# Kernel tuning notes

Measured on AMD Instinct MI355X. Metric: run time of the kernel, lower is better.

Reference implementation:

```python
import jax, jax.numpy as jnp
import numpy as np

B, T, I, H, L, C = 256, 128, 256, 1024, 2, 1000


def setup_inputs() -> dict:
    key = jax.random.key(0)
    ks = jax.random.split(key, 11)
    s_ih = 1.0 / np.sqrt(H)
    inp = {
        "x": jax.random.normal(ks[0], (B, T, I), dtype=jnp.float32),
        # layer 0: input_size -> hidden
        "Wih0": jax.random.uniform(ks[1], (H, I), jnp.float32, -s_ih, s_ih),
        "Whh0": jax.random.uniform(ks[2], (H, H), jnp.float32, -s_ih, s_ih),
        "bih0": jax.random.uniform(ks[3], (H,), jnp.float32, -s_ih, s_ih),
        "bhh0": jax.random.uniform(ks[4], (H,), jnp.float32, -s_ih, s_ih),
        # layer 1: hidden -> hidden
        "Wih1": jax.random.uniform(ks[5], (H, H), jnp.float32, -s_ih, s_ih),
        "Whh1": jax.random.uniform(ks[6], (H, H), jnp.float32, -s_ih, s_ih),
        "bih1": jax.random.uniform(ks[7], (H,), jnp.float32, -s_ih, s_ih),
        "bhh1": jax.random.uniform(ks[8], (H,), jnp.float32, -s_ih, s_ih),
        # fc head
        "fcW": jax.random.uniform(ks[9], (C, H), jnp.float32, -s_ih, s_ih),
        "fcb": jax.random.uniform(ks[10], (C,), jnp.float32, -s_ih, s_ih),
    }
    return inp


def _rnn_layer(x, Wih, Whh, bih, bhh):
    # x: [B, T, in]; h_t = tanh(x_t Wih^T + bih + h_{t-1} Whh^T + bhh)
    b, t, _ = x.shape
    h0 = jnp.zeros((b, Whh.shape[0]), dtype=x.dtype)
    # precompute input projection for all timesteps in one big GEMM
    xp = jnp.einsum('bti,hi->tbh', x, Wih) + (bih + bhh)  # [T, B, H]

    def step(h, xp_t):
        h_new = jnp.tanh(xp_t + h @ Whh.T)
        return h_new, h_new

    _, hs = jax.lax.scan(step, h0, xp)  # hs: [T, B, H]
    return jnp.transpose(hs, (1, 0, 2))  # [B, T, H]


def reference(x, Wih0, Whh0, bih0, bhh0, Wih1, Whh1, bih1, bhh1, fcW, fcb):
    x = jnp.reshape(x, (-1, T, I))
    h1 = _rnn_layer(x, Wih0, Whh0, bih0, bhh0)
    h2 = _rnn_layer(h1, Wih1, Whh1, bih1, bhh1)
    last = h2[:, -1, :]  # [B, H]
    return last @ fcW.T + fcb  # [B, C]
```

## Files before the change

kernel.cpp:

```cpp
#include <hip/hip_runtime.h>
#include <hip/hip_bf16.h>
#include <cstdint>
#include <cstddef>

typedef short v8s __attribute__((ext_vector_type(8)));
typedef float v4f __attribute__((ext_vector_type(4)));
typedef float v16f __attribute__((ext_vector_type(16)));

#define TT 128
#define BB 256
#define HH 1024
#define II 256
#define CC 1000

#define OFF_WHH0 0u
#define OFF_WHH1 1048576u
#define OFF_WIH1 2097152u
#define OFF_WIH0 3145728u
#define WSW_SHORTS 3407872u

#define NJ 32
#define CSTR 64
#define CNT_UINTS (12 * CSTR)
#define CNT_BYTES (CNT_UINTS * 4)

#define NCHUNK_LDS 50

__device__ __forceinline__ unsigned short f2bf(float f) {
  unsigned int u = __float_as_uint(f);
  u += 0x7fffu + ((u >> 16) & 1u);
  return (unsigned short)(u >> 16);
}
__device__ __forceinline__ float bf2f(unsigned short s) {
  return __uint_as_float((unsigned int)s << 16);
}
__device__ __forceinline__ float fast_tanh(float x) {
  float ax = fabsf(x);
  float e = __expf(-2.0f * ax);
  float r = 1.0f - 2.0f * e / (1.0f + e);
  return x < 0.0f ? -r : r;
}
__device__ __forceinline__ v16f mfma32(v8s a, v8s b, v16f c) {
  return __builtin_amdgcn_mfma_f32_32x32x16_bf16(a, b, c, 0, 0, 0);
}

__device__ __forceinline__ void poll_cnt(const unsigned int* p, unsigned int need) {
  while (__hip_atomic_load(p, __ATOMIC_RELAXED, __HIP_MEMORY_SCOPE_AGENT) < need)
    __builtin_amdgcn_s_sleep(1);
}
__device__ __forceinline__ void spin_tok(int* tok, int need) {
  while (__hip_atomic_load(tok, __ATOMIC_ACQUIRE, __HIP_MEMORY_SCOPE_WORKGROUP) < need) {}
  asm volatile("" ::: "memory");
}
__device__ __forceinline__ void set_tok(int* tok, int v) {
  __hip_atomic_store(tok, v, __ATOMIC_RELEASE, __HIP_MEMORY_SCOPE_WORKGROUP);
}
__device__ __forceinline__ void store16_llc(unsigned short* addr, v8s val) {
  asm volatile("global_store_dwordx4 %0, %1, off sc0 sc1"
               :: "v"(addr), "v"(val) : "memory");
}
__device__ __forceinline__ void waitcnt_vm0() {
  asm volatile("s_waitcnt vmcnt(0)" ::: "memory");
}

__global__ void swizzle_w(const float* __restrict__ W, unsigned short* __restrict__ out,
                          int K, int total) {
  int idx = blockIdx.x * 256 + threadIdx.x;
  if (idx >= total) return;
  int lane = idx & 63;
  int rest = idx >> 6;
  int KC = K >> 4;
  int kk = rest & (KC - 1);
  int jt = rest / KC;
  int row = jt * 32 + (lane & 31);
  int k0 = kk * 16 + (lane >> 5) * 8;
  const float* src = W + (size_t)row * K + k0;
  float4 f0 = *(const float4*)src;
  float4 f1 = *(const float4*)(src + 4);
  unsigned short o[8] = {f2bf(f0.x), f2bf(f0.y), f2bf(f0.z), f2bf(f0.w),
                         f2bf(f1.x), f2bf(f1.y), f2bf(f1.z), f2bf(f1.w)};
  *(v8s*)(out + (size_t)idx * 8) = *(const v8s*)o;
}

__global__ __launch_bounds__(256, 1) void xp_kernel(
    const float* __restrict__ x, const unsigned short* __restrict__ wih_sw,
    const float* __restrict__ bih0, const float* __restrict__ bhh0,
    unsigned short* __restrict__ xp) {
  __shared__ unsigned short lA[16 * 64 * 8];
  const int tid = threadIdx.x;
  const int lane = tid & 63, wave = tid >> 6;
  const int bi = blockIdx.x;
  const int t = bi >> 3, g = (bi >> 1) & 3, tile = bi & 1;
  const int b0 = g * 64 + tile * 32;
  #pragma unroll
  for (int s = 0; s < 4; ++s) {
    int idx = s * 256 + tid;
    int row = idx >> 5, kg = idx & 31;
    const float* src = x + ((size_t)(b0 + row) * TT + t) * II + kg * 8;
    float4 f0 = *(const float4*)src;
    float4 f1 = *(const float4*)(src + 4);
    unsigned short o[8] = {f2bf(f0.x), f2bf(f0.y), f2bf(f0.z), f2bf(f0.w),
                           f2bf(f1.x), f2bf(f1.y), f2bf(f1.z), f2bf(f1.w)};
    int kk = kg >> 1, hf = kg & 1;
    *(v8s*)(lA + ((size_t)kk * 64 + hf * 32 + row) * 8) = *(const v8s*)o;
  }
  __syncthreads();
  const int col = lane & 31;
  for (int jj = 0; jj < 8; ++jj) {
    int jt = wave * 8 + jj;
    float bias = bih0[jt * 32 + col] + bhh0[jt * 32 + col];
    v16f acc;
    #pragma unroll
    for (int r = 0; r < 16; ++r) acc[r] = bias;
    const unsigned short* bw = wih_sw + (size_t)jt * 8192;
    #pragma unroll 4
    for (int kk = 0; kk < 16; ++kk) {
      v8s a = *(const v8s*)(lA + ((size_t)kk * 64 + lane) * 8);
      v8s b = *(const v8s*)(bw + ((size_t)kk * 64 + lane) * 8);
      acc = mfma32(a, b, acc);
    }
    unsigned short o[16];
    #pragma unroll
    for (int r = 0; r < 16; ++r) o[r] = f2bf(acc[r]);
    unsigned short* dst = xp + ((size_t)((t * 4 + g) * 32 + jt) * 2 + tile) * 1024 + lane * 16;
    *(v8s*)dst = *(const v8s*)o;
    *(v8s*)(dst + 8) = *(const v8s*)(o + 8);
  }
}

template <int XPON, int BIGH2>
__global__ __launch_bounds__(256, 1) void rnn_fused(
    const float* __restrict__ x, const unsigned short* __restrict__ wsw,
    const unsigned short* __restrict__ xp,
    const float* __restrict__ bih0, const float* __restrict__ bhh0,
    const float* __restrict__ bih1, const float* __restrict__ bhh1,
    unsigned short* __restrict__ hbuf, unsigned short* __restrict__ h2buf,
    unsigned int* cnt) {
  __shared__ unsigned short lds_whh[NCHUNK_LDS * 512];
  __shared__ float lds_acc[2 * 1024];
  __shared__ unsigned short lds_pack[64 * 40];
  __shared__ int tok[4];

  const int tid = threadIdx.x;
  const int xsel = blockIdx.x & 7;
  const int layer = xsel >> 2;
  const int g = xsel & 3;
  const int jt = blockIdx.x >> 3;
  const int lane = tid & 63;
  const int wave = tid >> 6;
  const int tile = wave & 1;
  const int kh = wave >> 1;
  const int col = lane & 31;
  const int half = lane >> 5;
  const int j0 = jt * 32;

  const unsigned short* whh_tile =
      wsw + (layer ? OFF_WHH1 : OFF_WHH0) + (size_t)jt * 32768;
  const unsigned short* wih_tile =
      layer ? (wsw + OFF_WIH1 + (size_t)jt * 32768)
            : (wsw + OFF_WIH0 + (size_t)jt * 8192);

  for (int i = tid * 8; i < NCHUNK_LDS * 512; i += 2048)
    *(v8s*)(lds_whh + i) = *(const v8s*)(whh_tile + i);

  float bias = 0.0f;
  if (layer == 1) bias = bih1[j0 + col] + bhh1[j0 + col];
  else if (!XPON) bias = bih0[j0 + col] + bhh0[j0 + col];
  if (tid < 4) tok[tid] = 0;
  __syncthreads();

  const int arow = g * 64 + tile * 32 + col;
  unsigned int* cntA_g = cnt + (size_t)(0 * 4 + g) * CSTR;
  unsigned int* cntX_g = cnt + (size_t)(1 * 4 + g) * CSTR;
  unsigned int* cntB_g = cnt + (size_t)(2 * 4 + g) * CSTR;

  v8s xc0 = {}, xc1 = {};
  const unsigned short* xpb =
      xp + (((size_t)g * 32 + jt) * 2 + tile) * 1024 + lane * 16;
  if (XPON && layer == 0 && kh == 0) {
    xc0 = *(const v8s*)xpb;
    xc1 = *(const v8s*)(xpb + 8);
  }

  auto bL = [&](int kk) -> v8s {
    return *(const v8s*)(lds_whh + ((size_t)kk * 64 + lane) * 8);
  };
  auto bG = [&](int kk) -> v8s {
    return *(const v8s*)(whh_tile + ((size_t)kk * 64 + lane) * 8);
  };
  auto bI = [&](int kk) -> v8s {
    return *(const v8s*)(wih_tile + ((size_t)kk * 64 + lane) * 8);
  };

  for (int t = 0; t < TT; ++t) {
    v16f acc = {};

    if (layer == 0) {
      if (kh == 0) {
        if (XPON) {
          union { v8s v[2]; unsigned short u[16]; } xu;
          xu.v[0] = xc0; xu.v[1] = xc1;
          #pragma unroll
          for (int r = 0; r < 16; ++r) acc[r] = bf2f(xu.u[r]);
        } else {
          #pragma unroll
          for (int r = 0; r < 16; ++r) acc[r] = bias;
          const float* xr = x + ((size_t)arow * TT + t) * II + half * 8;
          #pragma unroll 4
          for (int kk = 0; kk < 16; ++kk) {
            float4 f0 = *(const float4*)(xr + kk * 16);
            float4 f1 = *(const float4*)(xr + kk * 16 + 4);
            unsigned short o[8] = {f2bf(f0.x), f2bf(f0.y), f2bf(f0.z), f2bf(f0.w),
                                   f2bf(f1.x), f2bf(f1.y), f2bf(f1.z), f2bf(f1.w)};
            acc = mfma32(*(const v8s*)o, bI(kk), acc);
          }
        }
        if (t > 0) {
          if (wave == 0) { poll_cnt(cntA_g, 32u * (unsigned)t); set_tok(&tok[0], t); }
          else           { spin_tok(&tok[0], t); }
          const unsigned short* hr = hbuf + ((size_t)t * BB + arow) * HH + half * 8;
          v8s aA[16], aB[16];
          #pragma unroll
          for (int kk = 0; kk < 16; ++kk) aA[kk] = *(const v8s*)(hr + kk * 16);
          #pragma unroll
          for (int kk = 0; kk < 16; ++kk) aB[kk] = *(const v8s*)(hr + (16 + kk) * 16);
          #pragma unroll
          for (int kk = 0; kk < 16; ++kk) acc = mfma32(aA[kk], bL(kk), acc);
          #pragma unroll
          for (int kk = 0; kk < 16; ++kk) acc = mfma32(aB[kk], bL(16 + kk), acc);
        }
        if (XPON) {
          int tn = (t + 1 < TT) ? (t + 1) : (TT - 1);
          const unsigned short* nx = xpb + (size_t)tn * 262144;
          xc0 = *(const v8s*)nx;
          xc1 = *(const v8s*)(nx + 8);
        }
      } else {
        if (t > 0) {
          spin_tok(&tok[0], t);
          const unsigned short* hr = hbuf + ((size_t)t * BB + arow) * HH + half * 8;
          v8s aA[16], aB[16];
          #pragma unroll
          for (int kk = 0; kk < 16; ++kk) aA[kk] = *(const v8s*)(hr + (32 + kk) * 16);
          #pragma unroll
          for (int kk = 0; kk < 16; ++kk) aB[kk] = *(const v8s*)(hr + (48 + kk) * 16);
          #pragma unroll
          for (int kk = 0; kk < 16; ++kk) {
            v8s b = (32 + kk < NCHUNK_LDS) ? bL(32 + kk) : bG(32 + kk);
            acc = mfma32(aA[kk], b, acc);
          }
          #pragma unroll
          for (int kk = 0; kk < 16; ++kk) {
            v8s b = (48 + kk < NCHUNK_LDS) ? bL(48 + kk) : bG(48 + kk);
            acc = mfma32(aB[kk], b, acc);
          }
        }
      }
    } else {
      if (kh == 0) {
        #pragma unroll
        for (int r = 0; r < 16; ++r) acc[r] = bias;
        if (wave == 0) { poll_cnt(cntX_g, 32u * (unsigned)(t + 1)); set_tok(&tok[1], t + 1); }
        else           { spin_tok(&tok[1], t + 1); }
        const unsigned short* hr = hbuf + ((size_t)(t + 1) * BB + arow) * HH + half * 8;
        v8s aA[16], aB[16];
        #pragma unroll
        for (int kk = 0; kk < 16; ++kk) aA[kk] = *(const v8s*)(hr + kk * 16);
        #pragma unroll
        for (int kk = 0; kk < 16; ++kk) aB[kk] = *(const v8s*)(hr + (16 + kk) * 16);
        #pragma unroll
        for (int kk = 0; kk < 16; ++kk) acc = mfma32(aA[kk], bI(kk), acc);
        #pragma unroll
        for (int kk = 0; kk < 16; ++kk) aA[kk] = *(const v8s*)(hr + (32 + kk) * 16);
        #pragma unroll
        for (int kk = 0; kk < 16; ++kk) acc = mfma32(aB[kk], bI(16 + kk), acc);
        #pragma unroll
        for (int kk = 0; kk < 16; ++kk) aB[kk] = *(const v8s*)(hr + (48 + kk) * 16);
        #pragma unroll
        for (int kk = 0; kk < 16; ++kk) acc = mfma32(aA[kk], bI(32 + kk), acc);
        #pragma unroll
        for (int kk = 0; kk < 16; ++kk) acc = mfma32(aB[kk], bI(48 + kk), acc);
      } else {
        if (t > 0) {
          if (wave == 2) { poll_cnt(cntB_g, 32u * (unsigned)t); set_tok(&tok[2], t); }
          else           { spin_tok(&tok[2], t); }
          const int slot_r = BIGH2 ? (t - 1) : ((t - 1) & 1);
          const unsigned short* hr =
              h2buf + ((size_t)slot_r * BB + arow) * HH + half * 8;
          if (BIGH2) {
            v8s aA[16], aB[16];
            #pragma unroll
            for (int kk = 0; kk < 16; ++kk) aA[kk] = *(const v8s*)(hr + kk * 16);
            #pragma unroll
            for (int kk = 0; kk < 16; ++kk) aB[kk] = *(const v8s*)(hr + (16 + kk) * 16);
            #pragma unroll
            for (int kk = 0; kk < 16; ++kk) acc = mfma32(aA[kk], bL(kk), acc);
            #pragma unroll
            for (int kk = 0; kk < 16; ++kk) aA[kk] = *(const v8s*)(hr + (32 + kk) * 16);
            #pragma unroll
            for (int kk = 0; kk < 16; ++kk) acc = mfma32(aB[kk], bL(16 + kk), acc);
            #pragma unroll
            for (int kk = 0; kk < 16; ++kk) aB[kk] = *(const v8s*)(hr + (48 + kk) * 16);
            #pragma unroll
            for (int kk = 0; kk < 16; ++kk) {
              v8s b = (32 + kk < NCHUNK_LDS) ? bL(32 + kk) : bG(32 + kk);
              acc = mfma32(aA[kk], b, acc);
            }
            #pragma unroll
            for (int kk = 0; kk < 16; ++kk) {
              v8s b = (48 + kk < NCHUNK_LDS) ? bL(48 + kk) : bG(48 + kk);
              acc = mfma32(aB[kk], b, acc);
            }
          } else {
            #pragma unroll 8
            for (int kk = 0; kk < 64; ++kk) {
              const unsigned long long* p = (const unsigned long long*)(hr + kk * 16);
              unsigned long long lo = __hip_atomic_load(p, __ATOMIC_RELAXED, __HIP_MEMORY_SCOPE_AGENT);
              unsigned long long hi = __hip_atomic_load(p + 1, __ATOMIC_RELAXED, __HIP_MEMORY_SCOPE_AGENT);
              union { unsigned long long q[2]; v8s v; } u;
              u.q[0] = lo; u.q[1] = hi;
              v8s b = (kk < NCHUNK_LDS) ? bL(kk) : bG(kk);
              acc = mfma32(u.v, b, acc);
            }
          }
        }
      }
    }

    if (kh == 1) {
      float* dst = lds_acc + tile * 1024;
      #pragma unroll
      for (int r4 = 0; r4 < 4; ++r4)
        *(float4*)(dst + r4 * 256 + lane * 4) =
            make_float4(acc[r4 * 4], acc[r4 * 4 + 1], acc[r4 * 4 + 2], acc[r4 * 4 + 3]);
    }
    __syncthreads();

    if (kh == 0) {
      const float* srcp = lds_acc + tile * 1024;
      #pragma unroll
      for (int r4 = 0; r4 < 4; ++r4) {
        float4 part = *(const float4*)(srcp + r4 * 256 + lane * 4);
        float pv[4] = {part.x, part.y, part.z, part.w};
        #pragma unroll
        for (int q = 0; q < 4; ++q) {
          int r = r4 * 4 + q;
          int row_l = tile * 32 + q + 8 * r4 + 4 * half;
          lds_pack[row_l * 40 + col] = f2bf(fast_tanh(acc[r] + pv[q]));
        }
      }
    }
    __syncthreads();

    {
      int row_l = tid >> 2, cg = tid & 3;
      v8s hv = *(const v8s*)(lds_pack + row_l * 40 + cg * 8);
      int slot_w = layer ? (BIGH2 ? t : (t & 1)) : (t + 1);
      unsigned short* hout = (layer ? h2buf : hbuf) +
          ((size_t)slot_w * BB + g * 64 + row_l) * HH + j0 + cg * 8;
      store16_llc(hout, hv);
    }
    waitcnt_vm0();
    __syncthreads();
    if (tid == 0) {
      if (layer == 0) {
        __hip_atomic_fetch_add(cntA_g, 1u, __ATOMIC_RELAXED, __HIP_MEMORY_SCOPE_AGENT);
        __hip_atomic_fetch_add(cntX_g, 1u, __ATOMIC_RELAXED, __HIP_MEMORY_SCOPE_AGENT);
      } else {
        __hip_atomic_fetch_add(cntB_g, 1u, __ATOMIC_RELAXED, __HIP_MEMORY_SCOPE_AGENT);
      }
    }
  }
}

__global__ __launch_bounds__(256, 1) void fc_kernel(
    const unsigned short* __restrict__ h2, const float* __restrict__ fcW,
    const float* __restrict__ fcb, float* __restrict__ out) {
  const int tid = threadIdx.x;
  const int ct = blockIdx.x % 63;
  const int g = blockIdx.x / 63;
  const int lane = tid & 63;
  const int wave = tid >> 6;
  const int n = lane & 15;
  const int quad = lane >> 4;
  const int c = ct * 16 + n;
  const int cs = c < CC ? c : CC - 1;
  const float bias = fcb[cs];
  v4f acc = {bias, bias, bias, bias};
  const unsigned short* hr = h2 + (size_t)(g * 64 + wave * 16 + n) * HH + quad * 8;
  const float* wr = fcW + (size_t)cs * HH + quad * 8;
  #pragma unroll 8
  for (int kk = 0; kk < HH / 32; ++kk) {
    v8s a = *(const v8s*)(hr + kk * 32);
    float4 f0 = *(const float4*)(wr + kk * 32);
    float4 f1 = *(const float4*)(wr + kk * 32 + 4);
    v8s b;
    b[0] = (short)f2bf(f0.x); b[1] = (short)f2bf(f0.y);
    b[2] = (short)f2bf(f0.z); b[3] = (short)f2bf(f0.w);
    b[4] = (short)f2bf(f1.x); b[5] = (short)f2bf(f1.y);
    b[6] = (short)f2bf(f1.z); b[7] = (short)f2bf(f1.w);
    acc = __builtin_amdgcn_mfma_f32_16x16x32_bf16(a, b, acc, 0, 0, 0);
  }
  if (c < CC) {
    const int b0 = g * 64 + wave * 16 + quad * 4;
    #pragma unroll
    for (int i = 0; i < 4; ++i) out[(size_t)(b0 + i) * CC + c] = acc[i];
  }
}

extern "C" void kernel_launch(void* const* d_in, const int* in_sizes, int n_in,
                              void* d_out, int out_size, void* d_ws, size_t ws_size,
                              hipStream_t stream) {
  (void)in_sizes; (void)n_in; (void)out_size;
  const float* x    = (const float*)d_in[0];
  const float* Wih0 = (const float*)d_in[1];
  const float* Whh0 = (const float*)d_in[2];
  const float* bih0 = (const float*)d_in[3];
  const float* bhh0 = (const float*)d_in[4];
  const float* Wih1 = (const float*)d_in[5];
  const float* Whh1 = (const float*)d_in[6];
  const float* bih1 = (const float*)d_in[7];
  const float* bhh1 = (const float*)d_in[8];
  const float* fcW  = (const float*)d_in[9];
  const float* fcb  = (const float*)d_in[10];

  const size_t hbuf_elems = (size_t)(TT + 1) * BB * HH;
  const size_t h2_full = (size_t)TT * BB * HH;
  const size_t h2_par  = (size_t)2 * BB * HH;
  const size_t xp_elems = (size_t)TT * BB * HH;

  const size_t needA = (WSW_SHORTS + hbuf_elems + h2_full + xp_elems) * 2 + CNT_BYTES;
  const size_t needB = (WSW_SHORTS + hbuf_elems + h2_par + xp_elems) * 2 + CNT_BYTES;
  const bool tierA = ws_size >= needA;
  const bool tierB = !tierA && ws_size >= needB;

  unsigned short* wsw = (unsigned short*)d_ws;
  unsigned short* hbuf = wsw + WSW_SHORTS;
  unsigned short* h2buf = hbuf + hbuf_elems;
  unsigned short* xpbuf = h2buf + (tierA ? h2_full : h2_par);
  unsigned int* cnt = (unsigned int*)(xpbuf + ((tierA || tierB) ? xp_elems : 0));

  hipMemsetAsync(cnt, 0, CNT_BYTES, stream);
  swizzle_w<<<512, 256, 0, stream>>>(Whh0, wsw + OFF_WHH0, HH, 32 * 64 * 64);
  swizzle_w<<<512, 256, 0, stream>>>(Whh1, wsw + OFF_WHH1, HH, 32 * 64 * 64);
  swizzle_w<<<512, 256, 0, stream>>>(Wih1, wsw + OFF_WIH1, HH, 32 * 64 * 64);
  swizzle_w<<<128, 256, 0, stream>>>(Wih0, wsw + OFF_WIH0, II, 32 * 16 * 64);

  if (tierA || tierB)
    xp_kernel<<<1024, 256, 0, stream>>>(x, wsw + OFF_WIH0, bih0, bhh0, xpbuf);

  if (tierA) {
    rnn_fused<1, 1><<<256, 256, 0, stream>>>(
        x, wsw, xpbuf, bih0, bhh0, bih1, bhh1, hbuf, h2buf, cnt);
  } else if (tierB) {
    rnn_fused<1, 0><<<256, 256, 0, stream>>>(
        x, wsw, xpbuf, bih0, bhh0, bih1, bhh1, hbuf, h2buf, cnt);
  } else {
    rnn_fused<0, 0><<<256, 256, 0, stream>>>(
        x, wsw, xpbuf, bih0, bhh0, bih1, bhh1, hbuf, h2buf, cnt);
  }

  const unsigned short* h2last = h2buf + (size_t)(tierA ? (TT - 1) : 1) * BB * HH;
  fc_kernel<<<63 * 4, 256, 0, stream>>>(h2last, fcW, fcb, (float*)d_out);
}
```

Measured before the change: 1.665 ms.

## Per-wave counter signaling, batched hidden-state loads, and sched_group_barrier MFMA interleave

```diff
diff --git a/kernel.cpp b/kernel.cpp
--- a/kernel.cpp
+++ b/kernel.cpp
@@ -25,6 +25,15 @@
 #define CNT_BYTES (CNT_UINTS * 4)
 
 #define NCHUNK_LDS 50
+
+#if defined(__has_builtin)
+#if __has_builtin(__builtin_amdgcn_sched_group_barrier)
+#define SGB(m, n) __builtin_amdgcn_sched_group_barrier((m), (n), 0)
+#endif
+#endif
+#ifndef SGB
+#define SGB(m, n)
+#endif
 
 __device__ __forceinline__ unsigned short f2bf(float f) {
   unsigned int u = __float_as_uint(f);
@@ -202,6 +211,10 @@
           xu.v[0] = xc0; xu.v[1] = xc1;
           #pragma unroll
           for (int r = 0; r < 16; ++r) acc[r] = bf2f(xu.u[r]);
+          int tn = (t + 1 < TT) ? (t + 1) : (TT - 1);
+          const unsigned short* nx = xpb + (size_t)tn * 262144;
+          xc0 = *(const v8s*)nx;
+          xc1 = *(const v8s*)(nx + 8);
         } else {
           #pragma unroll
           for (int r = 0; r < 16; ++r) acc[r] = bias;
@@ -216,101 +229,77 @@
           }
         }
         if (t > 0) {
-          if (wave == 0) { poll_cnt(cntA_g, 32u * (unsigned)t); set_tok(&tok[0], t); }
+          if (wave == 0) { poll_cnt(cntA_g, 128u * (unsigned)t); set_tok(&tok[0], t); }
           else           { spin_tok(&tok[0], t); }
           const unsigned short* hr = hbuf + ((size_t)t * BB + arow) * HH + half * 8;
-          v8s aA[16], aB[16];
-          #pragma unroll
-          for (int kk = 0; kk < 16; ++kk) aA[kk] = *(const v8s*)(hr + kk * 16);
-          #pragma unroll
-          for (int kk = 0; kk < 16; ++kk) aB[kk] = *(const v8s*)(hr + (16 + kk) * 16);
-          #pragma unroll
-          for (int kk = 0; kk < 16; ++kk) acc = mfma32(aA[kk], bL(kk), acc);
-          #pragma unroll
-          for (int kk = 0; kk < 16; ++kk) acc = mfma32(aB[kk], bL(16 + kk), acc);
-        }
-        if (XPON) {
-          int tn = (t + 1 < TT) ? (t + 1) : (TT - 1);
-          const unsigned short* nx = xpb + (size_t)tn * 262144;
-          xc0 = *(const v8s*)nx;
-          xc1 = *(const v8s*)(nx + 8);
+          v8s ar[32];
+          #pragma unroll
+          for (int kk = 0; kk < 32; ++kk) ar[kk] = *(const v8s*)(hr + kk * 16);
+          #pragma unroll
+          for (int kk = 0; kk < 32; ++kk) acc = mfma32(ar[kk], bL(kk), acc);
+          SGB(0x20, 32);
+          SGB(0x108, 64);
         }
       } else {
         if (t > 0) {
           spin_tok(&tok[0], t);
           const unsigned short* hr = hbuf + ((size_t)t * BB + arow) * HH + half * 8;
-          v8s aA[16], aB[16];
-          #pragma unroll
-          for (int kk = 0; kk < 16; ++kk) aA[kk] = *(const v8s*)(hr + (32 + kk) * 16);
-          #pragma unroll
-          for (int kk = 0; kk < 16; ++kk) aB[kk] = *(const v8s*)(hr + (48 + kk) * 16);
-          #pragma unroll
-          for (int kk = 0; kk < 16; ++kk) {
+          v8s ar[32];
+          #pragma unroll
+          for (int kk = 0; kk < 32; ++kk) ar[kk] = *(const v8s*)(hr + (32 + kk) * 16);
+          #pragma unroll
+          for (int kk = 0; kk < 32; ++kk) {
             v8s b = (32 + kk < NCHUNK_LDS) ? bL(32 + kk) : bG(32 + kk);
-            acc = mfma32(aA[kk], b, acc);
+            acc = mfma32(ar[kk], b, acc);
           }
-          #pragma unroll
-          for (int kk = 0; kk < 16; ++kk) {
-            v8s b = (48 + kk < NCHUNK_LDS) ? bL(48 + kk) : bG(48 + kk);
-            acc = mfma32(aB[kk], b, acc);
-          }
+          SGB(0x20, 46);
+          SGB(0x108, 50);
         }
       }
     } else {
       if (kh == 0) {
         #pragma unroll
         for (int r = 0; r < 16; ++r) acc[r] = bias;
-        if (wave == 0) { poll_cnt(cntX_g, 32u * (unsigned)(t + 1)); set_tok(&tok[1], t + 1); }
+        if (wave == 0) { poll_cnt(cntX_g, 128u * (unsigned)(t + 1)); set_tok(&tok[1], t + 1); }
         else           { spin_tok(&tok[1], t + 1); }
         const unsigned short* hr = hbuf + ((size_t)(t + 1) * BB + arow) * HH + half * 8;
-        v8s aA[16], aB[16];
-        #pragma unroll
-        for (int kk = 0; kk < 16; ++kk) aA[kk] = *(const v8s*)(hr + kk * 16);
-        #pragma unroll
-        for (int kk = 0; kk < 16; ++kk) aB[kk] = *(const v8s*)(hr + (16 + kk) * 16);
-        #pragma unroll
-        for (int kk = 0; kk < 16; ++kk) acc = mfma32(aA[kk], bI(kk), acc);
-        #pragma unroll
-        for (int kk = 0; kk < 16; ++kk) aA[kk] = *(const v8s*)(hr + (32 + kk) * 16);
-        #pragma unroll
-        for (int kk = 0; kk < 16; ++kk) acc = mfma32(aB[kk], bI(16 + kk), acc);
-        #pragma unroll
-        for (int kk = 0; kk < 16; ++kk) aB[kk] = *(const v8s*)(hr + (48 + kk) * 16);
-        #pragma unroll
-        for (int kk = 0; kk < 16; ++kk) acc = mfma32(aA[kk], bI(32 + kk), acc);
-        #pragma unroll
-        for (int kk = 0; kk < 16; ++kk) acc = mfma32(aB[kk], bI(48 + kk), acc);
+        v8s ar[32];
+        #pragma unroll
+        for (int kk = 0; kk < 32; ++kk) ar[kk] = *(const v8s*)(hr + kk * 16);
+        #pragma unroll
+        for (int kk = 0; kk < 32; ++kk) acc = mfma32(ar[kk], bI(kk), acc);
+        SGB(0x20, 64);
+        SGB(0x8, 32);
+        #pragma unroll
+        for (int kk = 0; kk < 32; ++kk) ar[kk] = *(const v8s*)(hr + (32 + kk) * 16);
+        #pragma unroll
+        for (int kk = 0; kk < 32; ++kk) acc = mfma32(ar[kk], bI(32 + kk), acc);
+        SGB(0x20, 64);
+        SGB(0x8, 32);
       } else {
         if (t > 0) {
-          if (wave == 2) { poll_cnt(cntB_g, 32u * (unsigned)t); set_tok(&tok[2], t); }
+          if (wave == 2) { poll_cnt(cntB_g, 128u * (unsigned)t); set_tok(&tok[2], t); }
           else           { spin_tok(&tok[2], t); }
           const int slot_r = BIGH2 ? (t - 1) : ((t - 1) & 1);
           const unsigned short* hr =
               h2buf + ((size_t)slot_r * BB + arow) * HH + half * 8;
           if (BIGH2) {
-            v8s aA[16], aB[16];
+            v8s ar[32];
             #pragma unroll
-            for (int kk = 0; kk < 16; ++kk) aA[kk] = *(const v8s*)(hr + kk * 16);
+            for (int kk = 0; kk < 32; ++kk) ar[kk] = *(const v8s*)(hr + kk * 16);
             #pragma unroll
-            for (int kk = 0; kk < 16; ++kk) aB[kk] = *(const v8s*)(hr + (16 + kk) * 16);
+            for (int kk = 0; kk < 32; ++kk) acc = mfma32(ar[kk], bL(kk), acc);
+            SGB(0x20, 32);
+            SGB(0x108, 64);
             #pragma unroll
-            for (int kk = 0; kk < 16; ++kk) acc = mfma32(aA[kk], bL(kk), acc);
+            for (int kk = 0; kk < 32; ++kk) ar[kk] = *(const v8s*)(hr + (32 + kk) * 16);
             #pragma unroll
-            for (int kk = 0; kk < 16; ++kk) aA[kk] = *(const v8s*)(hr + (32 + kk) * 16);
-            #pragma unroll
-            for (int kk = 0; kk < 16; ++kk) acc = mfma32(aB[kk], bL(16 + kk), acc);
-            #pragma unroll
-            for (int kk = 0; kk < 16; ++kk) aB[kk] = *(const v8s*)(hr + (48 + kk) * 16);
-            #pragma unroll
-            for (int kk = 0; kk < 16; ++kk) {
+            for (int kk = 0; kk < 32; ++kk) {
               v8s b = (32 + kk < NCHUNK_LDS) ? bL(32 + kk) : bG(32 + kk);
-              acc = mfma32(aA[kk], b, acc);
+              acc = mfma32(ar[kk], b, acc);
             }
-            #pragma unroll
-            for (int kk = 0; kk < 16; ++kk) {
-              v8s b = (48 + kk < NCHUNK_LDS) ? bL(48 + kk) : bG(48 + kk);
-              acc = mfma32(aB[kk], b, acc);
-            }
+            SGB(0x20, 46);
+            SGB(0x108, 50);
           } else {
             #pragma unroll 8
             for (int kk = 0; kk < 64; ++kk) {
@@ -361,8 +350,7 @@
       store16_llc(hout, hv);
     }
     waitcnt_vm0();
-    __syncthreads();
-    if (tid == 0) {
+    if (lane == 0) {
       if (layer == 0) {
         __hip_atomic_fetch_add(cntA_g, 1u, __ATOMIC_RELAXED, __HIP_MEMORY_SCOPE_AGENT);
         __hip_atomic_fetch_add(cntX_g, 1u, __ATOMIC_RELAXED, __HIP_MEMORY_SCOPE_AGENT);
@@ -370,6 +358,7 @@
         __hip_atomic_fetch_add(cntB_g, 1u, __ATOMIC_RELAXED, __HIP_MEMORY_SCOPE_AGENT);
       }
     }
+    __syncthreads();
   }
 }
 
```

After: 3.450 ms. 107% more time.

## Store hidden states in MFMA fragment-native layout for coalesced A-operand loads

Applied to the files above, without the earlier changes.

```diff
diff --git a/kernel.cpp b/kernel.cpp
--- a/kernel.cpp
+++ b/kernel.cpp
@@ -42,6 +42,10 @@
 }
 __device__ __forceinline__ v16f mfma32(v8s a, v8s b, v16f c) {
   return __builtin_amdgcn_mfma_f32_32x32x16_bf16(a, b, c, 0, 0, 0);
+}
+
+__device__ __forceinline__ size_t frag_off(int slot, int g, int tile) {
+  return ((((size_t)slot * 4 + g) * 2 + tile) << 15);
 }
 
 __device__ __forceinline__ void poll_cnt(const unsigned int* p, unsigned int need) {
@@ -218,12 +222,12 @@
         if (t > 0) {
           if (wave == 0) { poll_cnt(cntA_g, 32u * (unsigned)t); set_tok(&tok[0], t); }
           else           { spin_tok(&tok[0], t); }
-          const unsigned short* hr = hbuf + ((size_t)t * BB + arow) * HH + half * 8;
+          const unsigned short* hr = hbuf + frag_off(t, g, tile) + (size_t)lane * 8;
           v8s aA[16], aB[16];
           #pragma unroll
-          for (int kk = 0; kk < 16; ++kk) aA[kk] = *(const v8s*)(hr + kk * 16);
-          #pragma unroll
-          for (int kk = 0; kk < 16; ++kk) aB[kk] = *(const v8s*)(hr + (16 + kk) * 16);
+          for (int kk = 0; kk < 16; ++kk) aA[kk] = *(const v8s*)(hr + kk * 512);
+          #pragma unroll
+          for (int kk = 0; kk < 16; ++kk) aB[kk] = *(const v8s*)(hr + (16 + kk) * 512);
           #pragma unroll
           for (int kk = 0; kk < 16; ++kk) acc = mfma32(aA[kk], bL(kk), acc);
           #pragma unroll
@@ -238,12 +242,12 @@
       } else {
         if (t > 0) {
           spin_tok(&tok[0], t);
-          const unsigned short* hr = hbuf + ((size_t)t * BB + arow) * HH + half * 8;
+          const unsigned short* hr = hbuf + frag_off(t, g, tile) + (size_t)lane * 8;
           v8s aA[16], aB[16];
           #pragma unroll
-          for (int kk = 0; kk < 16; ++kk) aA[kk] = *(const v8s*)(hr + (32 + kk) * 16);
-          #pragma unroll
-          for (int kk = 0; kk < 16; ++kk) aB[kk] = *(const v8s*)(hr + (48 + kk) * 16);
+          for (int kk = 0; kk < 16; ++kk) aA[kk] = *(const v8s*)(hr + (32 + kk) * 512);
+          #pragma unroll
+          for (int kk = 0; kk < 16; ++kk) aB[kk] = *(const v8s*)(hr + (48 + kk) * 512);
           #pragma unroll
           for (int kk = 0; kk < 16; ++kk) {
             v8s b = (32 + kk < NCHUNK_LDS) ? bL(32 + kk) : bG(32 + kk);
@@ -262,20 +266,20 @@
         for (int r = 0; r < 16; ++r) acc[r] = bias;
         if (wave == 0) { poll_cnt(cntX_g, 32u * (unsigned)(t + 1)); set_tok(&tok[1], t + 1); }
         else           { spin_tok(&tok[1], t + 1); }
-        const unsigned short* hr = hbuf + ((size_t)(t + 1) * BB + arow) * HH + half * 8;
+        const unsigned short* hr = hbuf + frag_off(t + 1, g, tile) + (size_t)lane * 8;
         v8s aA[16], aB[16];
         #pragma unroll
-        for (int kk = 0; kk < 16; ++kk) aA[kk] = *(const v8s*)(hr + kk * 16);
-        #pragma unroll
-        for (int kk = 0; kk < 16; ++kk) aB[kk] = *(const v8s*)(hr + (16 + kk) * 16);
+        for (int kk = 0; kk < 16; ++kk) aA[kk] = *(const v8s*)(hr + kk * 512);
+        #pragma unroll
+        for (int kk = 0; kk < 16; ++kk) aB[kk] = *(const v8s*)(hr + (16 + kk) * 512);
         #pragma unroll
         for (int kk = 0; kk < 16; ++kk) acc = mfma32(aA[kk], bI(kk), acc);
         #pragma unroll
-        for (int kk = 0; kk < 16; ++kk) aA[kk] = *(const v8s*)(hr + (32 + kk) * 16);
+        for (int kk = 0; kk < 16; ++kk) aA[kk] = *(const v8s*)(hr + (32 + kk) * 512);
         #pragma unroll
         for (int kk = 0; kk < 16; ++kk) acc = mfma32(aB[kk], bI(16 + kk), acc);
         #pragma unroll
-        for (int kk = 0; kk < 16; ++kk) aB[kk] = *(const v8s*)(hr + (48 + kk) * 16);
+        for (int kk = 0; kk < 16; ++kk) aB[kk] = *(const v8s*)(hr + (48 + kk) * 512);
         #pragma unroll
         for (int kk = 0; kk < 16; ++kk) acc = mfma32(aA[kk], bI(32 + kk), acc);
         #pragma unroll
@@ -285,22 +289,21 @@
           if (wave == 2) { poll_cnt(cntB_g, 32u * (unsigned)t); set_tok(&tok[2], t); }
           else           { spin_tok(&tok[2], t); }
           const int slot_r = BIGH2 ? (t - 1) : ((t - 1) & 1);
-          const unsigned short* hr =
-              h2buf + ((size_t)slot_r * BB + arow) * HH + half * 8;
+          const unsigned short* hr = h2buf + frag_off(slot_r, g, tile) + (size_t)lane * 8;
           if (BIGH2) {
             v8s aA[16], aB[16];
             #pragma unroll
-            for (int kk = 0; kk < 16; ++kk) aA[kk] = *(const v8s*)(hr + kk * 16);
-            #pragma unroll
-            for (int kk = 0; kk < 16; ++kk) aB[kk] = *(const v8s*)(hr + (16 + kk) * 16);
+            for (int kk = 0; kk < 16; ++kk) aA[kk] = *(const v8s*)(hr + kk * 512);
+            #pragma unroll
+            for (int kk = 0; kk < 16; ++kk) aB[kk] = *(const v8s*)(hr + (16 + kk) * 512);
             #pragma unroll
             for (int kk = 0; kk < 16; ++kk) acc = mfma32(aA[kk], bL(kk), acc);
             #pragma unroll
-            for (int kk = 0; kk < 16; ++kk) aA[kk] = *(const v8s*)(hr + (32 + kk) * 16);
+            for (int kk = 0; kk < 16; ++kk) aA[kk] = *(const v8s*)(hr + (32 + kk) * 512);
             #pragma unroll
             for (int kk = 0; kk < 16; ++kk) acc = mfma32(aB[kk], bL(16 + kk), acc);
             #pragma unroll
-            for (int kk = 0; kk < 16; ++kk) aB[kk] = *(const v8s*)(hr + (48 + kk) * 16);
+            for (int kk = 0; kk < 16; ++kk) aB[kk] = *(const v8s*)(hr + (48 + kk) * 512);
             #pragma unroll
             for (int kk = 0; kk < 16; ++kk) {
               v8s b = (32 + kk < NCHUNK_LDS) ? bL(32 + kk) : bG(32 + kk);
@@ -314,7 +317,7 @@
           } else {
             #pragma unroll 8
             for (int kk = 0; kk < 64; ++kk) {
-              const unsigned long long* p = (const unsigned long long*)(hr + kk * 16);
+              const unsigned long long* p = (const unsigned long long*)(hr + kk * 512);
               unsigned long long lo = __hip_atomic_load(p, __ATOMIC_RELAXED, __HIP_MEMORY_SCOPE_AGENT);
               unsigned long long hi = __hip_atomic_load(p + 1, __ATOMIC_RELAXED, __HIP_MEMORY_SCOPE_AGENT);
               union { unsigned long long q[2]; v8s v; } u;
@@ -353,11 +356,13 @@
     __syncthreads();
 
     {
-      int row_l = tid >> 2, cg = tid & 3;
-      v8s hv = *(const v8s*)(lds_pack + row_l * 40 + cg * 8);
+      int tile_s = tid >> 7, kkl = (tid >> 6) & 1, flane = tid & 63;
+      v8s hv = *(const v8s*)(lds_pack +
+                             (tile_s * 32 + (flane & 31)) * 40 +
+                             kkl * 16 + (flane >> 5) * 8);
       int slot_w = layer ? (BIGH2 ? t : (t & 1)) : (t + 1);
       unsigned short* hout = (layer ? h2buf : hbuf) +
-          ((size_t)slot_w * BB + g * 64 + row_l) * HH + j0 + cg * 8;
+          frag_off(slot_w, g, tile_s) + ((size_t)(2 * jt + kkl) * 64 + flane) * 8;
       store16_llc(hout, hv);
     }
     waitcnt_vm0();
@@ -374,7 +379,7 @@
 }
 
 __global__ __launch_bounds__(256, 1) void fc_kernel(
-    const unsigned short* __restrict__ h2, const float* __restrict__ fcW,
+    const unsigned short* __restrict__ h2f, const float* __restrict__ fcW,
     const float* __restrict__ fcb, float* __restrict__ out) {
   const int tid = threadIdx.x;
   const int ct = blockIdx.x % 63;
@@ -387,11 +392,15 @@
   const int cs = c < CC ? c : CC - 1;
   const float bias = fcb[cs];
   v4f acc = {bias, bias, bias, bias};
-  const unsigned short* hr = h2 + (size_t)(g * 64 + wave * 16 + n) * HH + quad * 8;
+  const int brow = wave * 16 + n;
+  const int tile = brow >> 5;
+  const int flane = (brow & 31) + 32 * (quad & 1);
+  const unsigned short* hb = h2f + (((size_t)g * 2 + tile) << 15) + (size_t)flane * 8;
   const float* wr = fcW + (size_t)cs * HH + quad * 8;
   #pragma unroll 8
   for (int kk = 0; kk < HH / 32; ++kk) {
-    v8s a = *(const v8s*)(hr + kk * 32);
+    int c2 = kk * 2 + (quad >> 1);
+    v8s a = *(const v8s*)(hb + (size_t)c2 * 512);
     float4 f0 = *(const float4*)(wr + kk * 32);
     float4 f1 = *(const float4*)(wr + kk * 32 + 4);
     v8s b;
@@ -460,6 +469,7 @@
         x, wsw, xpbuf, bih0, bhh0, bih1, bhh1, hbuf, h2buf, cnt);
   }
 
-  const unsigned short* h2last = h2buf + (size_t)(tierA ? (TT - 1) : 1) * BB * HH;
+  const unsigned short* h2last =
+      h2buf + (size_t)(tierA ? (TT - 1) : 1) * BB * HH;
   fc_kernel<<<63 * 4, 256, 0, stream>>>(h2last, fcW, fcb, (float*)d_out);
 }
```

Measured after the change: 1.399 ms. 16.0% less time.
